# Kernel optimization log

Measured on AMD Instinct MI355X. Metric: run time of the kernel, lower is better.

Reference implementation:

```python
import jax, jax.numpy as jnp
import numpy as np

H, D, K = 8, 64, 9           # new num heads, head size, conv kernel size
A = H * D                    # all_head_size = 512
HID = 2 * A                  # input hidden size = 1024
STD = 0.02


def setup_inputs() -> dict:
    key = jax.random.key(0)
    ks = jax.random.split(key, 16)
    B, S = 4, 2048
    f = jnp.float32
    inp = {
        'hidden_states': jax.random.normal(ks[0], (B, S, HID), f),
        'Wq': jax.random.normal(ks[1], (A, A), f) * STD,
        'bq': jnp.zeros((A,), f),
        'Wk': jax.random.normal(ks[2], (A, A), f) * STD,
        'bk': jnp.zeros((A,), f),
        'Wv': jax.random.normal(ks[3], (A, A), f) * STD,
        'bv': jnp.zeros((A,), f),
        'dw_w': jax.random.normal(ks[4], (A, 1, K), f) * STD,   # depthwise conv (groups=A)
        'pw_w': jax.random.normal(ks[5], (A, A, 1), f) * STD,   # pointwise 1x1 conv
        'sep_b': jnp.zeros((A, 1), f),                          # SeparableConv1D bias
        'Wck': jax.random.normal(ks[6], (H * K, A), f) * STD,   # conv_kernel_layer
        'bck': jnp.zeros((H * K,), f),
        'Wco': jax.random.normal(ks[7], (A, A), f) * STD,       # conv_out_layer
        'bco': jnp.zeros((A,), f),
    }
    return inp


def reference(hidden_states, Wq, bq, Wk, bk, Wv, bv, dw_w, pw_w, sep_b, Wck, bck, Wco, bco):
    B, S, _ = hidden_states.shape
    hs_attn = hidden_states[:, :, :A]
    hs_conv = hidden_states[:, :, A:]

    q = hs_attn @ Wq.T + bq
    k = hs_attn @ Wk.T + bk
    v = hs_attn @ Wv.T + bv

    # SeparableConv1D on (B, A, S): depthwise then pointwise, plus bias
    x = hs_conv.transpose(0, 2, 1)
    x = jax.lax.conv_general_dilated(
        x, dw_w, window_strides=(1,), padding=[(K // 2, K // 2)],
        feature_group_count=A, dimension_numbers=('NCH', 'OIH', 'NCH'))
    x = jnp.einsum('bcs,oc->bos', x, pw_w[:, :, 0]) + sep_b
    mixed_key_conv = x.transpose(0, 2, 1)            # (B,S,A)

    # per-token softmax conv kernel
    conv_attn = mixed_key_conv * hs_conv
    ckl = (conv_attn @ Wck.T + bck).reshape(B, S, H, K)
    ckl = jax.nn.softmax(ckl, axis=-1)               # softmax over kernel taps

    # dynamic-span lightweight convolution (unfold -> batched matmul)
    col = hs_conv @ Wco.T + bco                      # (B,S,A)
    pad = jnp.pad(col, ((0, 0), (K // 2, K // 2), (0, 0)))
    windows = jnp.stack([pad[:, i:i + S] for i in range(K)], axis=-1)  # (B,S,A,K)
    windows = windows.reshape(B, S, H, D, K)
    conv_out = jnp.einsum('bshdk,bshk->bshd', windows, ckl)            # (B,S,H,D)

    # standard self-attention
    qh = q.reshape(B, S, H, D).transpose(0, 2, 1, 3)
    kh = k.reshape(B, S, H, D).transpose(0, 2, 1, 3)
    vh = v.reshape(B, S, H, D).transpose(0, 2, 1, 3)
    scale = jnp.asarray(1.0 / np.sqrt(D), q.dtype)
    scores = jnp.einsum('bhqd,bhkd->bhqk', qh, kh) * scale
    probs = jax.nn.softmax(scores, axis=-1)
    ctx = jnp.einsum('bhqk,bhkd->bqhd', probs, vh)   # (B,S,H,D)

    out = jnp.concatenate([ctx, conv_out], axis=2)   # (B,S,2H,D)
    return out.reshape(B, S, HID)
```

## Files before the change

### kernel.cpp

```cpp
#include <hip/hip_runtime.h>
#include <hip/hip_bf16.h>

#define NH   8
#define HD   64
#define KW   9
#define AD   512
#define HIDD 1024
#define BB   4
#define SS   2048
#define MTOK (BB*SS)
#define WSZ  262144

typedef __attribute__((ext_vector_type(8))) short short8;
typedef __attribute__((ext_vector_type(4))) float floatx4;
typedef __attribute__((ext_vector_type(16))) float floatx16;

__device__ __forceinline__ short f2bf(float f) {
    unsigned u = __float_as_uint(f);
    u = (u + 0x7FFFu + ((u >> 16) & 1u)) >> 16;
    return (short)u;
}
__device__ __forceinline__ float bf2f(short s) {
    return __uint_as_float(((unsigned)(unsigned short)s) << 16);
}
__device__ __forceinline__ float exp2_raw(float x) {
    return __builtin_amdgcn_exp2f(x);
}
__device__ __forceinline__ unsigned pkbf2(float a, float b) {
    unsigned d;
    asm("v_cvt_pk_bf16_f32 %0, %1, %2" : "=v"(d) : "v"(a), "v"(b));
    return d;
}
__device__ __forceinline__ void gl2lds16(const short* g, short* l) {
    __builtin_amdgcn_global_load_lds(
        (const __attribute__((address_space(1))) void*)g,
        (__attribute__((address_space(3))) void*)l, 16, 0, 0);
}

__global__ __launch_bounds__(256) void prep_kernel(
    const float* __restrict__ hs,
    const float* __restrict__ pw, const float* __restrict__ Wco,
    const float* __restrict__ Wq, const float* __restrict__ Wk,
    const float* __restrict__ Wv, const float* __restrict__ Wck,
    const float* __restrict__ dw,
    short* __restrict__ hsb, short* __restrict__ wb, short* __restrict__ x1)
{
    __shared__ float wl[KW * AD];
    const int bid = blockIdx.x, tid = threadIdx.x;

    if (bid < 4096) {
        int idx = bid * 256 + tid;
        const float* s = hs + (long)idx * 8;
        float4 a = *(const float4*)s, c = *(const float4*)(s + 4);
        short8 o;
        o[0]=f2bf(a.x); o[1]=f2bf(a.y); o[2]=f2bf(a.z); o[3]=f2bf(a.w);
        o[4]=f2bf(c.x); o[5]=f2bf(c.y); o[6]=f2bf(c.z); o[7]=f2bf(c.w);
        *(short8*)(hsb + (long)idx * 8) = o;
    } else if (bid < 4768) {
        int idx = (bid - 4096) * 256 + tid;
        int e0 = idx * 8;
        short8 o;
        if (e0 < 5 * WSZ) {
            int w = e0 >> 18, off = e0 & (WSZ - 1);
            const float* src = (w == 0) ? pw : (w == 1) ? Wco : (w == 2) ? Wq
                             : (w == 3) ? Wk : Wv;
            float4 a = *(const float4*)(src + off), c = *(const float4*)(src + off + 4);
            o[0]=f2bf(a.x); o[1]=f2bf(a.y); o[2]=f2bf(a.z); o[3]=f2bf(a.w);
            o[4]=f2bf(c.x); o[5]=f2bf(c.y); o[6]=f2bf(c.z); o[7]=f2bf(c.w);
        } else {
            int off = e0 - 5 * WSZ;
            int row = off >> 9, col = off & 511;
            if (row < NH * KW) {
                const float* src = Wck + row * AD + col;
                float4 a = *(const float4*)src, c = *(const float4*)(src + 4);
                o[0]=f2bf(a.x); o[1]=f2bf(a.y); o[2]=f2bf(a.z); o[3]=f2bf(a.w);
                o[4]=f2bf(c.x); o[5]=f2bf(c.y); o[6]=f2bf(c.z); o[7]=f2bf(c.w);
            } else {
                for (int i = 0; i < 8; ++i) o[i] = 0;
            }
        }
        *(short8*)(wb + e0) = o;
    } else {
        for (int t = tid; t < KW * AD; t += 256) {
            int c = t / KW, k = t - c * KW;
            wl[k * AD + c] = dw[t];
        }
        __syncthreads();
        int idx = (bid - 4768) * 256 + tid;
        int c8  = (idx & 63) * 8;
        int tok = idx >> 6;
        int s   = tok & (SS - 1);
        int b   = tok >> 11;
        const float* base = hs + (long)(b * SS) * HIDD + AD + c8;
        float acc[8];
#pragma unroll
        for (int i = 0; i < 8; ++i) acc[i] = 0.f;
#pragma unroll
        for (int kk = 0; kk < KW; ++kk) {
            int ss2 = s + kk - KW / 2;
            if (ss2 >= 0 && ss2 < SS) {
                const float* hp = base + (long)ss2 * HIDD;
                float4 h0 = *(const float4*)hp;
                float4 h1 = *(const float4*)(hp + 4);
                float4 w0 = *(const float4*)(wl + kk * AD + c8);
                float4 w1 = *(const float4*)(wl + kk * AD + c8 + 4);
                acc[0] += w0.x * h0.x; acc[1] += w0.y * h0.y;
                acc[2] += w0.z * h0.z; acc[3] += w0.w * h0.w;
                acc[4] += w1.x * h1.x; acc[5] += w1.y * h1.y;
                acc[6] += w1.z * h1.z; acc[7] += w1.w * h1.w;
            }
        }
        short8 o;
#pragma unroll
        for (int i = 0; i < 8; ++i) o[i] = f2bf(acc[i]);
        *(short8*)(x1 + (long)tok * AD + c8) = o;
    }
}

template<int FM, int FN, int MODE>
__device__ __forceinline__ void gemm_body(
    int bx, int by, short* As, short* Bs,
    const short* __restrict__ X, int ldx, int xoff,
    const short* __restrict__ W,
    const float* __restrict__ b0p, const float* __restrict__ b1p,
    const float* __restrict__ b2p,
    const short* __restrict__ mulp, int mul_ld, int mul_off,
    void* __restrict__ Cout, short* __restrict__ vtout,
    int ldc, int N, int Kd, float oscale)
{
    constexpr int TM = 32 * FM, TN = 32 * FN;
    const int tid  = threadIdx.x;
    const int wv   = tid >> 6, lane = tid & 63;
    const int ln   = lane & 15, quad = lane >> 4;
    const int wm   = wv >> 1, wn = wv & 1;
    const int m0 = bx * TM, n0 = by * TN;

    floatx4 acc[FM][FN];
#pragma unroll
    for (int i = 0; i < FM; ++i)
#pragma unroll
        for (int j = 0; j < FN; ++j) acc[i][j] = (floatx4){0.f, 0.f, 0.f, 0.f};

    const short* xbase = X + (long)m0 * ldx + xoff;
    const short* wbase = W + (long)n0 * Kd;

    for (int k0 = 0; k0 < Kd; k0 += 64) {
#pragma unroll
        for (int g = tid; g < TM * 8; g += 256) {
            int m = g >> 3, p = g & 7, gk = p ^ (m & 7);
            gl2lds16(xbase + (long)m * ldx + k0 + gk * 8, &As[g * 8]);
        }
#pragma unroll
        for (int g = tid; g < TN * 8; g += 256) {
            int m = g >> 3, p = g & 7, gk = p ^ (m & 7);
            gl2lds16(wbase + (long)m * Kd + k0 + gk * 8, &Bs[g * 8]);
        }
        __syncthreads();
#pragma unroll
        for (int half = 0; half < 2; ++half) {
            short8 afr[FM], bfr[FN];
#pragma unroll
            for (int i = 0; i < FM; ++i) {
                int p = (half * 4 + quad) ^ (ln & 7);
                afr[i] = *(const short8*)&As[(wm * 16 * FM + i * 16 + ln) * 64 + p * 8];
            }
#pragma unroll
            for (int j = 0; j < FN; ++j) {
                int p = (half * 4 + quad) ^ (ln & 7);
                bfr[j] = *(const short8*)&Bs[(wn * 16 * FN + j * 16 + ln) * 64 + p * 8];
            }
#pragma unroll
            for (int i = 0; i < FM; ++i)
#pragma unroll
                for (int j = 0; j < FN; ++j)
                    acc[i][j] = __builtin_amdgcn_mfma_f32_16x16x32_bf16(
                        afr[i], bfr[j], acc[i][j], 0, 0, 0);
        }
        __syncthreads();
    }

#pragma unroll
    for (int j = 0; j < FN; ++j) {
        int n = n0 + wn * 16 * FN + j * 16 + ln;
        if constexpr (MODE == 3) {
            if (n >= 1024) {
                int hh = (n - 1024) >> 6, dd = (n - 1024) & 63;
                float bv = b2p[n - 1024];
                int mblk = m0 + wm * 16 * FM;
                int bidx = mblk >> 11, sblk = mblk & (SS - 1);
                short* dst = vtout + ((long)((bidx * NH + hh) * HD + dd)) * SS + sblk;
#pragma unroll
                for (int i = 0; i < FM; ++i) {
                    unsigned lo = pkbf2(acc[i][j][0] + bv, acc[i][j][1] + bv);
                    unsigned hi = pkbf2(acc[i][j][2] + bv, acc[i][j][3] + bv);
                    *(uint2*)(dst + i * 16 + quad * 4) = make_uint2(lo, hi);
                }
            } else {
                float bv = (n < 512) ? b0p[n] : b1p[n - 512];
                float sc = (n < 512) ? oscale : 1.f;
#pragma unroll
                for (int i = 0; i < FM; ++i) {
#pragma unroll
                    for (int r = 0; r < 4; ++r) {
                        int m = m0 + wm * 16 * FM + i * 16 + quad * 4 + r;
                        float val = (acc[i][j][r] + bv) * sc;
                        ((short*)Cout)[(long)m * ldc + n] = f2bf(val);
                    }
                }
            }
        } else if (n < N) {
            float bv = b0p[n], sc = oscale;
#pragma unroll
            for (int i = 0; i < FM; ++i) {
#pragma unroll
                for (int r = 0; r < 4; ++r) {
                    int m = m0 + wm * 16 * FM + i * 16 + quad * 4 + r;
                    float val = (acc[i][j][r] + bv) * sc;
                    if constexpr (MODE == 2)
                        val *= bf2f(mulp[(long)m * mul_ld + mul_off + n]);
                    if constexpr (MODE == 0)
                        ((float*)Cout)[(long)m * ldc + n] = val;
                    else
                        ((short*)Cout)[(long)m * ldc + n] = f2bf(val);
                }
            }
        }
    }
}

__global__ __launch_bounds__(256) void mega1_kernel(
    const short* __restrict__ hsb, const short* __restrict__ x1c,
    const short* __restrict__ Wqkv_b, const short* __restrict__ pw_b,
    const float* __restrict__ bq, const float* __restrict__ bk,
    const float* __restrict__ bv, const float* __restrict__ sepb,
    short* __restrict__ qkvb, short* __restrict__ vTb,
    short* __restrict__ cabO, float oscale)
{
    __shared__ __align__(16) short As[128 * 64];
    __shared__ __align__(16) short Bs[128 * 64];
    int bid = blockIdx.x;
    if (bid < 768) {
        gemm_body<4, 4, 3>(bid & 63, bid >> 6, As, Bs,
            hsb, HIDD, 0, Wqkv_b, bq, bk, bv, nullptr, 0, 0,
            qkvb, vTb, 1536, 1536, AD, oscale);
    } else {
        int id = bid - 768;
        gemm_body<4, 4, 2>(id & 63, id >> 6, As, Bs,
            x1c, AD, 0, pw_b, sepb, nullptr, nullptr, hsb, HIDD, AD,
            cabO, nullptr, 2048, AD, AD, 1.f);
    }
}

__global__ __launch_bounds__(256) void mega3_kernel(
    const short* __restrict__ qkv, const short* __restrict__ vT,
    const short* __restrict__ hsb, const short* __restrict__ cabO,
    const short* __restrict__ Wco_b, const short* __restrict__ Wck_b,
    const float* __restrict__ bco, const float* __restrict__ bck,
    short* __restrict__ x1c, float* __restrict__ cklp,
    float* __restrict__ out)
{
    __shared__ __align__(16) char smem[49664];
    const int bid = blockIdx.x;
    const int tid = threadIdx.x;

    if (bid >= 512) {
        short* As = (short*)smem;
        short* Bs = (short*)smem + 128 * 64;
        if (bid < 768) {
            int id = bid - 512;
            gemm_body<4, 4, 1>(id & 63, id >> 6, As, Bs,
                hsb, HIDD, AD, Wco_b, bco, nullptr, nullptr, nullptr, 0, 0,
                x1c, nullptr, AD, AD, AD, 1.f);
        } else {
            int id = bid - 768;
            gemm_body<2, 2, 0>(id & 127, id >> 7, As, Bs,
                cabO, 2048, 0, Wck_b, bck, nullptr, nullptr, nullptr, 0, 0,
                cklp, nullptr, NH * KW, NH * KW, AD, 1.f);
        }
        return;
    }

    short* const KbB = (short*)smem;
    short* const VbB = (short*)smem + 3 * 4096;
    float* const ls  = (float*)(smem + 49152);

    const int qt = bid & 15, h = (bid >> 4) & 7, b = bid >> 7;
    const int w    = tid >> 6;
    const int lane = tid & 63;
    const int l5   = lane & 31;
    const int hh   = lane >> 5;

    const int  q0 = qt * 128 + w * 32;
    const long rowbase = (long)b * SS;

    short8 qf[4];
    {
        const short* qrow = qkv + (rowbase + q0 + l5) * 1536 + h * HD;
#pragma unroll
        for (int i = 0; i < 4; ++i)
            qf[i] = *(const short8*)(qrow + i * 16 + hh * 8);
    }

    floatx16 acc0, acc1;
    floatx16 Z;
#pragma unroll
    for (int r = 0; r < 16; ++r) { acc0[r] = 0.f; acc1[r] = 0.f; Z[r] = 0.f; }
    float l_i = 0.f;

    const int m1 = tid >> 3,  gk1 = (tid & 7) ^ (m1 & 7);
    const int g2 = 256 + tid;
    const int m2 = g2 >> 3,   gk2 = (g2 & 7) ^ (m2 & 7);
    const short* kbase  = qkv + 512 + rowbase * 1536 + h * HD;
    const short* vtbase = vT + ((long)(b * NH + h) * HD) * SS;
    const short* sk0 = kbase  + (long)m1 * 1536 + gk1 * 8;
    const short* sk1 = kbase  + (long)m2 * 1536 + gk2 * 8;
    const short* sv0 = vtbase + (long)m1 * SS   + gk1 * 8;
    const short* sv1 = vtbase + (long)m2 * SS   + gk2 * 8;

    auto STAGE_K = [&](int slot, bool adv) {
        gl2lds16(sk0, KbB + slot * 4096 + tid * 8);
        gl2lds16(sk1, KbB + slot * 4096 + g2 * 8);
        if (adv) { sk0 += 64 * 1536; sk1 += 64 * 1536; }
    };
    auto STAGE_V = [&](int slot) {
        gl2lds16(sv0, VbB + slot * 4096 + tid * 8);
        gl2lds16(sv1, VbB + slot * 4096 + g2 * 8);
        sv0 += 64; sv1 += 64;
    };

    auto qkt = [&](const short* KB, floatx16& S0, floatx16& S1) {
        {
            int p = hh ^ (l5 & 7);
            short8 k0 = *(const short8*)&KB[l5 * 64 + p * 8];
            short8 k1 = *(const short8*)&KB[(32 + l5) * 64 + p * 8];
            S0 = __builtin_amdgcn_mfma_f32_32x32x16_bf16(k0, qf[0], Z, 0, 0, 0);
            S1 = __builtin_amdgcn_mfma_f32_32x32x16_bf16(k1, qf[0], Z, 0, 0, 0);
        }
#pragma unroll
        for (int i = 1; i < 4; ++i) {
            int p = (2 * i + hh) ^ (l5 & 7);
            short8 k0 = *(const short8*)&KB[l5 * 64 + p * 8];
            short8 k1 = *(const short8*)&KB[(32 + l5) * 64 + p * 8];
            S0 = __builtin_amdgcn_mfma_f32_32x32x16_bf16(k0, qf[i], S0, 0, 0, 0);
            S1 = __builtin_amdgcn_mfma_f32_32x32x16_bf16(k1, qf[i], S1, 0, 0, 0);
        }
    };

    auto smax = [&](const floatx16& S0, const floatx16& S1, short8* pf) {
        float pe0[16], pe1[16];
#pragma unroll
        for (int r = 0; r < 16; ++r) {
            pe0[r] = exp2_raw(S0[r]);
            pe1[r] = exp2_raw(S1[r]);
        }
        float s = 0.f;
#pragma unroll
        for (int r = 0; r < 16; ++r) s += pe0[r] + pe1[r];
        l_i += s;
#pragma unroll
        for (int t = 0; t < 2; ++t) {
            const float* pe = t ? pe1 : pe0;
#pragma unroll
            for (int u = 0; u < 2; ++u) {
                unsigned a0 = pkbf2(pe[8 * u + 0], pe[8 * u + 1]);
                unsigned a1 = pkbf2(pe[8 * u + 2], pe[8 * u + 3]);
                unsigned b0 = pkbf2(pe[8 * u + 4], pe[8 * u + 5]);
                unsigned b1 = pkbf2(pe[8 * u + 6], pe[8 * u + 7]);
                asm("v_permlane32_swap_b32 %0, %1" : "+v"(a0), "+v"(b0));
                asm("v_permlane32_swap_b32 %0, %1" : "+v"(a1), "+v"(b1));
                union { uint4 u4; short8 s8; } cv;
                cv.u4 = make_uint4(a0, a1, b0, b1);
                pf[t * 2 + u] = cv.s8;
            }
        }
    };

    auto pv = [&](const short* VB, const short8* pf) {
#pragma unroll
        for (int s = 0; s < 4; ++s) {
            int p = (2 * s + hh) ^ (l5 & 7);
            short8 v0 = *(const short8*)&VB[l5 * 64 + p * 8];
            short8 v1 = *(const short8*)&VB[(32 + l5) * 64 + p * 8];
            acc0 = __builtin_amdgcn_mfma_f32_32x32x16_bf16(pf[s], v0, acc0, 0, 0, 0);
            acc1 = __builtin_amdgcn_mfma_f32_32x32x16_bf16(pf[s], v1, acc1, 0, 0, 0);
        }
    };

    short8 pfA[4], pfB[4];

    STAGE_K(0, true);
    STAGE_K(1, true);
    STAGE_V(0);
    asm volatile("s_waitcnt vmcnt(0)" ::: "memory");
    __builtin_amdgcn_s_barrier();
    asm volatile("" ::: "memory");

    {
        STAGE_K(2, true);
        STAGE_V(1);
        floatx16 S0, S1;
        qkt(KbB, S0, S1);
        smax(S0, S1, pfA);
        asm volatile("s_waitcnt vmcnt(4)" ::: "memory");
        __builtin_amdgcn_s_barrier();
        asm volatile("" ::: "memory");
    }

#define PHASE(KS, VPS, KST, VST, KADV, PIN, POUT)                      \
    {                                                                  \
        STAGE_K(KST, KADV);                                            \
        STAGE_V(VST);                                                  \
        floatx16 S0, S1;                                               \
        __builtin_amdgcn_s_setprio(1);                                 \
        qkt(KbB + (KS) * 4096, S0, S1);                                \
        pv(VbB + (VPS) * 4096, PIN);                                   \
        __builtin_amdgcn_s_setprio(0);                                 \
        smax(S0, S1, POUT);                                            \
        asm volatile("s_waitcnt vmcnt(4)" ::: "memory");               \
        __builtin_amdgcn_s_barrier();                                  \
        asm volatile("" ::: "memory");                                 \
    }

    for (int g = 0; g < 5; ++g) {
        bool notlast = (g < 4);
        PHASE(1, 0, 0, 2, true,    pfA, pfB);
        PHASE(2, 1, 1, 0, true,    pfB, pfA);
        PHASE(0, 2, 2, 1, true,    pfA, pfB);
        PHASE(1, 0, 0, 2, true,    pfB, pfA);
        PHASE(2, 1, 1, 0, notlast, pfA, pfB);
        PHASE(0, 2, 2, 1, notlast, pfB, pfA);
    }
#undef PHASE

    {
        floatx16 S0, S1;
        __builtin_amdgcn_s_setprio(1);
        qkt(KbB + 1 * 4096, S0, S1);
        pv(VbB + 0 * 4096, pfA);
        __builtin_amdgcn_s_setprio(0);
        smax(S0, S1, pfB);
        asm volatile("s_waitcnt vmcnt(0)" ::: "memory");
        __builtin_amdgcn_s_barrier();
        asm volatile("" ::: "memory");
    }
    pv(VbB + 1 * 4096, pfB);

    l_i += __shfl_xor(l_i, 32);
    ls[w * 32 + l5] = 1.f / l_i;
    float4 lv[4];
#pragma unroll
    for (int g = 0; g < 4; ++g)
        lv[g] = *(const float4*)&ls[w * 32 + 8 * g + 4 * hh];

#pragma unroll
    for (int r = 0; r < 16; ++r) {
        int g = r >> 2, j = r & 3;
        int qr = j + 8 * g + 4 * hh;
        float iv = lv[g][j];
        float* orow = out + (rowbase + q0 + qr) * HIDD + h * HD;
        orow[l5]      = acc0[r] * iv;
        orow[32 + l5] = acc1[r] * iv;
    }
}

__global__ __launch_bounds__(256) void convout_kernel(
    const short* __restrict__ col, const float* __restrict__ ckl,
    float* __restrict__ out)
{
    int idx = blockIdx.x * 256 + threadIdx.x;
    int d4  = (idx & 127) * 4;
    int tok = idx >> 7;
    int s   = tok & (SS - 1);
    int b   = tok >> 11;
    int h   = d4 >> 6;
    const float* lg = ckl + (long)tok * (NH * KW) + h * KW;
    float wv[KW];
    float mx = -1e30f;
#pragma unroll
    for (int i = 0; i < KW; ++i) { wv[i] = lg[i]; mx = fmaxf(mx, wv[i]); }
    float sum = 0.f;
#pragma unroll
    for (int i = 0; i < KW; ++i) { wv[i] = __expf(wv[i] - mx); sum += wv[i]; }
    float inv = 1.f / sum;
    float a0 = 0.f, a1 = 0.f, a2 = 0.f, a3 = 0.f;
    const short* cbase = col + (long)(b * SS) * AD + d4;
#pragma unroll
    for (int kk = 0; kk < KW; ++kk) {
        int ss2 = s + kk - KW / 2;
        if (ss2 >= 0 && ss2 < SS) {
            uint2 cv = *(const uint2*)(cbase + (long)ss2 * AD);
            float w = wv[kk];
            a0 += w * bf2f((short)(cv.x & 0xFFFF));
            a1 += w * bf2f((short)(cv.x >> 16));
            a2 += w * bf2f((short)(cv.y & 0xFFFF));
            a3 += w * bf2f((short)(cv.y >> 16));
        }
    }
    *(float4*)&out[(long)tok * HIDD + AD + d4] =
        make_float4(a0 * inv, a1 * inv, a2 * inv, a3 * inv);
}

extern "C" void kernel_launch(void* const* d_in, const int* in_sizes, int n_in,
                              void* d_out, int out_size, void* d_ws, size_t ws_size,
                              hipStream_t stream)
{
    const float* hs   = (const float*)d_in[0];
    const float* Wq   = (const float*)d_in[1];
    const float* bq   = (const float*)d_in[2];
    const float* Wk   = (const float*)d_in[3];
    const float* bk   = (const float*)d_in[4];
    const float* Wv   = (const float*)d_in[5];
    const float* bv   = (const float*)d_in[6];
    const float* dw   = (const float*)d_in[7];
    const float* pw   = (const float*)d_in[8];
    const float* sepb = (const float*)d_in[9];
    const float* Wck  = (const float*)d_in[10];
    const float* bck  = (const float*)d_in[11];
    const float* Wco  = (const float*)d_in[12];
    const float* bco  = (const float*)d_in[13];
    float* out = (float*)d_out;

    short* hsb  = (short*)d_ws;
    short* x1c  = hsb + (long)MTOK * HIDD;
    short* qkvb = x1c + (long)MTOK * AD;
    short* vTb  = qkvb + (long)MTOK * 1536;
    float* ckl  = (float*)(vTb + (long)MTOK * AD);
    short* wb   = (short*)(ckl + (long)MTOK * (NH * KW));
    short* pw_b   = wb;
    short* Wco_b  = wb + 1L * WSZ;
    short* Wqkv_b = wb + 2L * WSZ;
    short* Wck_b  = wb + 5L * WSZ;
    short* cabO   = (short*)d_out + 1024;

    const float QSCALE = 0.18033688011112042f;

    prep_kernel<<<6816, 256, 0, stream>>>(
        hs, pw, Wco, Wq, Wk, Wv, Wck, dw, hsb, wb, x1c);
    mega1_kernel<<<1024, 256, 0, stream>>>(
        hsb, x1c, Wqkv_b, pw_b, bq, bk, bv, sepb, qkvb, vTb, cabO, QSCALE);
    mega3_kernel<<<1024, 256, 0, stream>>>(
        qkvb, vTb, hsb, cabO, Wco_b, Wck_b, bco, bck, x1c, ckl, out);
    convout_kernel<<<MTOK * AD / 1024, 256, 0, stream>>>(x1c, ckl, out);

    (void)in_sizes; (void)n_in; (void)out_size; (void)ws_size;
}
```

Baseline: 211.6 us.

## Double-buffer GEMM LDS tiles, shrink N tiles, and widen convout vectors

The shared GEMM body now uses two LDS slots. It prefetches the next K-tile through direct global-to-LDS loads while MFMAs run on the current one, cutting one barrier per iteration. The pointwise and Wco GEMMs switch to 128x64 tiles to raise block count, and the launch grids grow to match. The convout kernel now processes 8 channels per thread with 16-byte loads. The cost is more LDS per block (64 KB in mega1), which may lower occupancy.

```diff
diff --git a/kernel.cpp b/kernel.cpp
--- a/kernel.cpp
+++ b/kernel.cpp
@@ -119,7 +119,7 @@
 
 template<int FM, int FN, int MODE>
 __device__ __forceinline__ void gemm_body(
-    int bx, int by, short* As, short* Bs,
+    int bx, int by, short* Sm,
     const short* __restrict__ X, int ldx, int xoff,
     const short* __restrict__ W,
     const float* __restrict__ b0p, const float* __restrict__ b1p,
@@ -129,6 +129,7 @@
     int ldc, int N, int Kd, float oscale)
 {
     constexpr int TM = 32 * FM, TN = 32 * FN;
+    constexpr int SLOT = (TM + TN) * 64;
     const int tid  = threadIdx.x;
     const int wv   = tid >> 6, lane = tid & 63;
     const int ln   = lane & 15, quad = lane >> 4;
@@ -144,7 +145,9 @@
     const short* xbase = X + (long)m0 * ldx + xoff;
     const short* wbase = W + (long)n0 * Kd;
 
-    for (int k0 = 0; k0 < Kd; k0 += 64) {
+    auto stage = [&](int k0, int slot) {
+        short* As = Sm + slot * SLOT;
+        short* Bs = As + TM * 64;
 #pragma unroll
         for (int g = tid; g < TM * 8; g += 256) {
             int m = g >> 3, p = g & 7, gk = p ^ (m & 7);
@@ -155,7 +158,10 @@
             int m = g >> 3, p = g & 7, gk = p ^ (m & 7);
             gl2lds16(wbase + (long)m * Kd + k0 + gk * 8, &Bs[g * 8]);
         }
-        __syncthreads();
+    };
+    auto compute = [&](int slot) {
+        const short* As = Sm + slot * SLOT;
+        const short* Bs = As + TM * 64;
 #pragma unroll
         for (int half = 0; half < 2; ++half) {
             short8 afr[FM], bfr[FN];
@@ -176,8 +182,24 @@
                     acc[i][j] = __builtin_amdgcn_mfma_f32_16x16x32_bf16(
                         afr[i], bfr[j], acc[i][j], 0, 0, 0);
         }
-        __syncthreads();
-    }
+    };
+
+    stage(0, 0);
+    asm volatile("s_waitcnt vmcnt(0)" ::: "memory");
+    __builtin_amdgcn_s_barrier();
+    asm volatile("" ::: "memory");
+
+    const int nk = Kd >> 6;
+    int slot = 0;
+    for (int t = 0; t < nk - 1; ++t) {
+        stage((t + 1) * 64, slot ^ 1);
+        compute(slot);
+        asm volatile("s_waitcnt vmcnt(0)" ::: "memory");
+        __builtin_amdgcn_s_barrier();
+        asm volatile("" ::: "memory");
+        slot ^= 1;
+    }
+    compute(slot);
 
 #pragma unroll
     for (int j = 0; j < FN; ++j) {
@@ -236,16 +258,15 @@
     short* __restrict__ qkvb, short* __restrict__ vTb,
     short* __restrict__ cabO, float oscale)
 {
-    __shared__ __align__(16) short As[128 * 64];
-    __shared__ __align__(16) short Bs[128 * 64];
+    __shared__ __align__(16) char smem[65536];
     int bid = blockIdx.x;
     if (bid < 768) {
-        gemm_body<4, 4, 3>(bid & 63, bid >> 6, As, Bs,
+        gemm_body<4, 4, 3>(bid & 63, bid >> 6, (short*)smem,
             hsb, HIDD, 0, Wqkv_b, bq, bk, bv, nullptr, 0, 0,
             qkvb, vTb, 1536, 1536, AD, oscale);
     } else {
         int id = bid - 768;
-        gemm_body<4, 4, 2>(id & 63, id >> 6, As, Bs,
+        gemm_body<4, 2, 2>(id & 63, id >> 6, (short*)smem,
             x1c, AD, 0, pw_b, sepb, nullptr, nullptr, hsb, HIDD, AD,
             cabO, nullptr, 2048, AD, AD, 1.f);
     }
@@ -264,16 +285,14 @@
     const int tid = threadIdx.x;
 
     if (bid >= 512) {
-        short* As = (short*)smem;
-        short* Bs = (short*)smem + 128 * 64;
-        if (bid < 768) {
+        if (bid < 1024) {
             int id = bid - 512;
-            gemm_body<4, 4, 1>(id & 63, id >> 6, As, Bs,
+            gemm_body<4, 2, 1>(id & 63, id >> 6, (short*)smem,
                 hsb, HIDD, AD, Wco_b, bco, nullptr, nullptr, nullptr, 0, 0,
                 x1c, nullptr, AD, AD, AD, 1.f);
         } else {
-            int id = bid - 768;
-            gemm_body<2, 2, 0>(id & 127, id >> 7, As, Bs,
+            int id = bid - 1024;
+            gemm_body<2, 2, 0>(id & 127, id >> 7, (short*)smem,
                 cabO, 2048, 0, Wck_b, bck, nullptr, nullptr, nullptr, 0, 0,
                 cklp, nullptr, NH * KW, NH * KW, AD, 1.f);
         }
@@ -468,11 +487,11 @@
     float* __restrict__ out)
 {
     int idx = blockIdx.x * 256 + threadIdx.x;
-    int d4  = (idx & 127) * 4;
-    int tok = idx >> 7;
+    int d8  = (idx & 63) * 8;
+    int tok = idx >> 6;
     int s   = tok & (SS - 1);
     int b   = tok >> 11;
-    int h   = d4 >> 6;
+    int h   = d8 >> 6;
     const float* lg = ckl + (long)tok * (NH * KW) + h * KW;
     float wv[KW];
     float mx = -1e30f;
@@ -482,22 +501,29 @@
 #pragma unroll
     for (int i = 0; i < KW; ++i) { wv[i] = __expf(wv[i] - mx); sum += wv[i]; }
     float inv = 1.f / sum;
-    float a0 = 0.f, a1 = 0.f, a2 = 0.f, a3 = 0.f;
-    const short* cbase = col + (long)(b * SS) * AD + d4;
+    float a[8];
+#pragma unroll
+    for (int i = 0; i < 8; ++i) a[i] = 0.f;
+    const short* cbase = col + (long)(b * SS) * AD + d8;
 #pragma unroll
     for (int kk = 0; kk < KW; ++kk) {
         int ss2 = s + kk - KW / 2;
         if (ss2 >= 0 && ss2 < SS) {
-            uint2 cv = *(const uint2*)(cbase + (long)ss2 * AD);
+            uint4 cv = *(const uint4*)(cbase + (long)ss2 * AD);
             float w = wv[kk];
-            a0 += w * bf2f((short)(cv.x & 0xFFFF));
-            a1 += w * bf2f((short)(cv.x >> 16));
-            a2 += w * bf2f((short)(cv.y & 0xFFFF));
-            a3 += w * bf2f((short)(cv.y >> 16));
-        }
-    }
-    *(float4*)&out[(long)tok * HIDD + AD + d4] =
-        make_float4(a0 * inv, a1 * inv, a2 * inv, a3 * inv);
+            a[0] += w * bf2f((short)(cv.x & 0xFFFF));
+            a[1] += w * bf2f((short)(cv.x >> 16));
+            a[2] += w * bf2f((short)(cv.y & 0xFFFF));
+            a[3] += w * bf2f((short)(cv.y >> 16));
+            a[4] += w * bf2f((short)(cv.z & 0xFFFF));
+            a[5] += w * bf2f((short)(cv.z >> 16));
+            a[6] += w * bf2f((short)(cv.w & 0xFFFF));
+            a[7] += w * bf2f((short)(cv.w >> 16));
+        }
+    }
+    float* op = &out[(long)tok * HIDD + AD + d8];
+    *(float4*)op       = make_float4(a[0]*inv, a[1]*inv, a[2]*inv, a[3]*inv);
+    *(float4*)(op + 4) = make_float4(a[4]*inv, a[5]*inv, a[6]*inv, a[7]*inv);
 }
 
 extern "C" void kernel_launch(void* const* d_in, const int* in_sizes, int n_in,
@@ -536,11 +562,11 @@
 
     prep_kernel<<<6816, 256, 0, stream>>>(
         hs, pw, Wco, Wq, Wk, Wv, Wck, dw, hsb, wb, x1c);
-    mega1_kernel<<<1024, 256, 0, stream>>>(
+    mega1_kernel<<<1280, 256, 0, stream>>>(
         hsb, x1c, Wqkv_b, pw_b, bq, bk, bv, sepb, qkvb, vTb, cabO, QSCALE);
-    mega3_kernel<<<1024, 256, 0, stream>>>(
+    mega3_kernel<<<1280, 256, 0, stream>>>(
         qkvb, vTb, hsb, cabO, Wco_b, Wck_b, bco, bck, x1c, ckl, out);
-    convout_kernel<<<MTOK * AD / 1024, 256, 0, stream>>>(x1c, ckl, out);
+    convout_kernel<<<MTOK * AD / 2048, 256, 0, stream>>>(x1c, ckl, out);
 
     (void)in_sizes; (void)n_in; (void)out_size; (void)ws_size;
 }
```

Result: no change. 207.9 us (-1.8%).
